# Performance work log

Measured on AMD Instinct MI355X. Metric: run time of the kernel, lower is better.

The kernel has to match this reference:

```python
import jax, jax.numpy as jnp
import numpy as np

N_NODES = 50000
N_EDGES = 800000
C_IN = 32          # in_channels
N_RAD = 8          # num_radial gaussians
RBF_START, RBF_STOP = 0.0, 5.0


def setup_inputs() -> dict:
    key = jax.random.key(0)
    ks = jax.random.split(key, 8)
    x = jax.random.normal(ks[0], (N_NODES, C_IN), dtype=jnp.float32)
    pos = jax.random.normal(ks[1], (N_NODES, 3), dtype=jnp.float32)
    edge_index = jax.random.randint(ks[2], (2, N_EDGES), 0, N_NODES, dtype=jnp.int64)
    # Xavier-uniform-style init for weights
    def xavier(k, shape, fan_in, fan_out):
        lim = np.sqrt(6.0 / (fan_in + fan_out))
        return jax.random.uniform(k, shape, minval=-lim, maxval=lim, dtype=jnp.float32)
    W_tp = xavier(ks[3], (C_IN, N_RAD, C_IN), C_IN, N_RAD * C_IN)
    W1 = xavier(ks[4], (N_RAD * C_IN, C_IN), N_RAD * C_IN, C_IN)
    b1 = jnp.zeros((C_IN,), dtype=jnp.float32)
    W2 = xavier(ks[5], (C_IN, C_IN), C_IN, C_IN)
    b2 = jnp.zeros((C_IN,), dtype=jnp.float32)
    return {"x": x, "pos": pos, "edge_index": edge_index,
            "W_tp": W_tp, "W1": W1, "b1": b1, "W2": W2, "b2": b2}


def _gaussian_smearing(dist):
    # dist: (E,) -> (E, N_RAD)
    centers = jnp.linspace(RBF_START, RBF_STOP, N_RAD)  # (R,)
    width = (RBF_STOP - RBF_START) / (N_RAD - 1)
    scaling = 1.0 / jnp.sqrt(2.0 * jnp.pi)
    d = dist[:, None] - centers[None, :]
    return scaling * jnp.exp(-0.5 * (d / width) ** 2)


def reference(x, pos, edge_index, W_tp, W1, b1, W2, b2):
    row = edge_index[0]  # target (central) nodes
    col = edge_index[1]  # source (neighbor) nodes
    # edge geometry
    edge_vector = pos[row] - pos[col]                       # (E, 3)
    dist = jnp.sqrt(jnp.sum(edge_vector * edge_vector, axis=-1) + 1e-12)  # (E,)
    rbf = _gaussian_smearing(dist)                          # (E, R)
    # tensor product: gather neighbor features, weight by radial basis
    x_j = x[col]                                            # (E, C)
    weighted = jnp.einsum('ec,cro->ero', x_j, W_tp)         # (E, R, C)
    tp = weighted * rbf[:, :, None]                         # (E, R, C)
    # per-edge MLP on flattened tensor-product output
    msg = tp.reshape(tp.shape[0], -1)                       # (E, R*C)
    msg = jax.nn.silu(msg @ W1 + b1)                        # (E, C)
    msg = msg @ W2 + b2                                     # (E, C)
    # scatter-add messages to central nodes, residual update
    agg = jax.ops.segment_sum(msg, row, num_segments=x.shape[0])  # (N, C)
    return x + agg
```

## Files before the change

kernel.cpp:

```cpp
#include <hip/hip_runtime.h>
#include <hip/hip_bf16.h>

#define C 32
#define R 8
#define NPB 32
#define K_ELL 32
#define OVF_CAP 65536

typedef unsigned int u32;
__device__ __forceinline__ float bflo(u32 u) { return __uint_as_float(u << 16); }
__device__ __forceinline__ float bfhi(u32 u) { return __uint_as_float(u & 0xffff0000u); }
__device__ __forceinline__ u32 f2bf_bits(float f) {
    u32 u = __float_as_uint(f);
    u32 lsb = (u >> 16) & 1u;
    return (u + 0x7fffu + lsb) >> 16;
}

__global__ void k_prepM(const float* __restrict__ Wtp, const float* __restrict__ W1,
                        float* __restrict__ M) {
    int idx = blockIdx.x * 256 + threadIdx.x;
    if (idx >= R * C * C) return;
    int r = idx >> 10;
    int c = (idx >> 5) & 31;
    int j = idx & 31;
    float acc = 0.f;
#pragma unroll
    for (int o = 0; o < C; ++o)
        acc = fmaf(Wtp[c * R * C + r * C + o], W1[(r * C + o) * C + j], acc);
    M[idx] = acc;
}

__global__ void k_fused(const float* __restrict__ x, const float* __restrict__ M,
                        __hip_bfloat16* __restrict__ z,
                        const int* __restrict__ ei, const float* __restrict__ pos,
                        int* __restrict__ cnt, int* __restrict__ ovfcnt,
                        uint4* __restrict__ ovf,
                        u32* __restrict__ ell, int N, int E, int ZB) {
    __shared__ float xs[NPB * C];
    int t = threadIdx.x;
    if ((int)blockIdx.x < ZB) {
        int n0 = blockIdx.x * NPB;
        for (int i = t * 4; i < NPB * C; i += 256 * 4) {
            size_t gbase = (size_t)n0 * C + i;
            float4 v = make_float4(0.f, 0.f, 0.f, 0.f);
            if (gbase + 3 < (size_t)N * C) v = *(const float4*)(x + gbase);
            *(float4*)(xs + i) = v;
        }
        __syncthreads();
        int r = t & 7, j = t >> 3;
        float m[C];
#pragma unroll
        for (int c = 0; c < C; ++c) m[c] = M[r * C * C + c * C + j];
        int nmax = N - n0; if (nmax > NPB) nmax = NPB;
        for (int nn = 0; nn < nmax; ++nn) {
            const float* xp = xs + nn * C;
            float acc = 0.f;
#pragma unroll
            for (int c = 0; c < C; ++c) acc = fmaf(xp[c], m[c], acc);
            z[(size_t)(n0 + nn) * (R * C) + t] = __float2bfloat16(acc);
        }
    } else {
        int i = (blockIdx.x - ZB) * 256 + t;
        if (i < E) {
            int r = ei[i];
            int c = ei[E + i];
            r = ((unsigned)r < (unsigned)N) ? r : 0;
            c = ((unsigned)c < (unsigned)N) ? c : 0;
            float dx = pos[r * 3 + 0] - pos[c * 3 + 0];
            float dy = pos[r * 3 + 1] - pos[c * 3 + 1];
            float dz = pos[r * 3 + 2] - pos[c * 3 + 2];
            float dist = sqrtf(fmaf(dx, dx, fmaf(dy, dy, dz * dz)) + 1e-12f);
            int local = atomicAdd(&cnt[r], 1);
            if (local < K_ELL) {
                ell[(size_t)r * K_ELL + local] = (u32)c | (f2bf_bits(dist) << 16);
            } else {
                int q = atomicAdd(ovfcnt, 1);
                if (q < OVF_CAP)
                    ovf[q] = make_uint4((u32)r, (u32)c, __float_as_uint(dist), 0u);
            }
        }
    }
}

__device__ __forceinline__ float silu_f(float h) {
    return h * __builtin_amdgcn_rcpf(1.f + __expf(-h));
}

__device__ __forceinline__ float rbf_dot(float d, uint4 zv, float b1j) {
    const float Einv = 0.36787944f;
    float u = 1.3999999f * d;
    float f = 0.3989423f * __expf(-0.5f * u * u);
    float t = __expf(u - 0.5f);
    float h = fmaf(f, bflo(zv.x), b1j);
    f *= t;            h = fmaf(f, bfhi(zv.x), h);
    t *= Einv; f *= t; h = fmaf(f, bflo(zv.y), h);
    t *= Einv; f *= t; h = fmaf(f, bfhi(zv.y), h);
    t *= Einv; f *= t; h = fmaf(f, bflo(zv.z), h);
    t *= Einv; f *= t; h = fmaf(f, bfhi(zv.z), h);
    t *= Einv; f *= t; h = fmaf(f, bflo(zv.w), h);
    t *= Einv; f *= t; h = fmaf(f, bfhi(zv.w), h);
    return h;
}

__global__ void k_edge_ell(const int* __restrict__ cnt, const u32* __restrict__ ell,
                           const __hip_bfloat16* __restrict__ z,
                           const float* __restrict__ x, const float* __restrict__ b1,
                           const float* __restrict__ W2, const float* __restrict__ b2,
                           float* __restrict__ out, int N) {
    __shared__ float W2s[C * C];
    for (int i = threadIdx.x; i < C * C; i += blockDim.x) W2s[i] = W2[i];
    __syncthreads();
    int gt = blockIdx.x * blockDim.x + threadIdx.x;
    int j = gt & 31;
    int n = gt >> 5;
    if (n >= N) return;
    int deg = cnt[n];
    int m = deg < K_ELL ? deg : K_ELL;
    u32 packv = 0u;
    if (j < m) packv = ell[(size_t)n * K_ELL + j];
    float b1j = b1[j];
    float acc = 0.f;
    int base = 0;
    for (; base + 4 <= m; base += 4) {
        u32 w0 = __shfl(packv, base + 0, 32);
        u32 w1 = __shfl(packv, base + 1, 32);
        u32 w2 = __shfl(packv, base + 2, 32);
        u32 w3 = __shfl(packv, base + 3, 32);
        uint4 z0 = ((const uint4*)(z + (size_t)(w0 & 0xffffu) * (R * C)))[j];
        uint4 z1 = ((const uint4*)(z + (size_t)(w1 & 0xffffu) * (R * C)))[j];
        uint4 z2 = ((const uint4*)(z + (size_t)(w2 & 0xffffu) * (R * C)))[j];
        uint4 z3 = ((const uint4*)(z + (size_t)(w3 & 0xffffu) * (R * C)))[j];
        float h0 = rbf_dot(__uint_as_float(w0 & 0xffff0000u), z0, b1j);
        float h1 = rbf_dot(__uint_as_float(w1 & 0xffff0000u), z1, b1j);
        float h2 = rbf_dot(__uint_as_float(w2 & 0xffff0000u), z2, b1j);
        float h3 = rbf_dot(__uint_as_float(w3 & 0xffff0000u), z3, b1j);
        acc += silu_f(h0) + silu_f(h1) + silu_f(h2) + silu_f(h3);
    }
    for (; base < m; ++base) {
        u32 w0 = __shfl(packv, base, 32);
        uint4 z0 = ((const uint4*)(z + (size_t)(w0 & 0xffffu) * (R * C)))[j];
        acc += silu_f(rbf_dot(__uint_as_float(w0 & 0xffff0000u), z0, b1j));
    }
    float v = fmaf((float)deg, b2[j], x[(size_t)n * C + j]);
#pragma unroll
    for (int i = 0; i < C; ++i)
        v = fmaf(__shfl(acc, i, 32), W2s[i * C + j], v);
    out[(size_t)n * C + j] = v;
}

__global__ void k_overflow(const int* __restrict__ ovfcnt, const uint4* __restrict__ ovf,
                           const __hip_bfloat16* __restrict__ z,
                           const float* __restrict__ b1, const float* __restrict__ W2,
                           float* __restrict__ out, int N) {
    int novf = ovfcnt[0];
    if (novf > OVF_CAP) novf = OVF_CAP;
    int gt = blockIdx.x * blockDim.x + threadIdx.x;
    int j = gt & 31;
    int g = gt >> 5;
    int ngroups = (gridDim.x * blockDim.x) >> 5;
    for (int q = g; q < novf; q += ngroups) {
        uint4 rec = ovf[q];
        u32 row = rec.x, col = rec.y;
        float dist = __uint_as_float(rec.z);
        uint4 zv = ((const uint4*)(z + (size_t)col * (R * C)))[j];
        float sh = silu_f(rbf_dot(dist, zv, b1[j]));
        float v = 0.f;
#pragma unroll
        for (int i = 0; i < C; ++i)
            v = fmaf(__shfl(sh, i, 32), W2[i * C + j], v);
        atomicAdd(&out[(size_t)row * C + j], v);
    }
}

__device__ __forceinline__ float rbf_lane(float dist, int r) {
    float t = (dist - 0.71428573f * (float)r) * 1.3999999f;
    return 0.3989423f * __expf(-0.5f * t * t);
}

__global__ void k_edge_direct(const int* __restrict__ ei, const float* __restrict__ pos,
                              const float* __restrict__ x, const float* __restrict__ M,
                              const float* __restrict__ b1,
                              float* __restrict__ agg, float* __restrict__ deg,
                              int E, int N) {
    __shared__ float Ms[R * C * C];
    for (int i = threadIdx.x; i < R * C * C; i += blockDim.x) Ms[i] = M[i];
    __syncthreads();
    int gt = blockIdx.x * blockDim.x + threadIdx.x;
    int j = gt & 31;
    int g = gt >> 5;
    int ngroups = (gridDim.x * blockDim.x) >> 5;
    float b1j = b1[j];
    for (int e = g; e < E; e += ngroups) {
        int row = ei[e];
        int col = ei[E + e];
        row = ((unsigned)row < (unsigned)N) ? row : 0;
        col = ((unsigned)col < (unsigned)N) ? col : 0;
        float dx = pos[row * 3 + 0] - pos[col * 3 + 0];
        float dy = pos[row * 3 + 1] - pos[col * 3 + 1];
        float dz = pos[row * 3 + 2] - pos[col * 3 + 2];
        float dist = sqrtf(fmaf(dx, dx, fmaf(dy, dy, dz * dz)) + 1e-12f);
        float my_rbf = rbf_lane(dist, j & 7);
        float xr[C];
#pragma unroll
        for (int c = 0; c < C; ++c) xr[c] = x[(size_t)col * C + c];
        float h = b1j;
#pragma unroll
        for (int r = 0; r < R; ++r) {
            float s = 0.f;
#pragma unroll
            for (int c = 0; c < C; ++c)
                s = fmaf(xr[c], Ms[r * C * C + c * C + j], s);
            h = fmaf(__shfl(my_rbf, r, 32), s, h);
        }
        float sh = h / (1.f + __expf(-h));
        atomicAdd(&agg[(size_t)row * C + j], sh);
        if (j == 0) atomicAdd(&deg[row], 1.f);
    }
}

__global__ void k_final(const float* __restrict__ x, const float* __restrict__ agg,
                        const float* __restrict__ deg, const float* __restrict__ W2,
                        const float* __restrict__ b2, float* __restrict__ out,
                        int N) {
    int t = threadIdx.x;
    int j = t & 31;
    float w2[C];
#pragma unroll
    for (int i = 0; i < C; ++i) w2[i] = W2[i * C + j];
    float b2j = b2[j];
    int g = (blockIdx.x * blockDim.x + t) >> 5;
    int ngroups = (gridDim.x * blockDim.x) >> 5;
    for (int n = g; n < N; n += ngroups) {
        const float* ap = agg + (size_t)n * C;
        float acc = 0.f;
#pragma unroll
        for (int i = 0; i < C; ++i) acc = fmaf(ap[i], w2[i], acc);
        out[(size_t)n * C + j] = x[(size_t)n * C + j] + acc + deg[n] * b2j;
    }
}

__global__ void k_edge_full(const int* __restrict__ ei, const float* __restrict__ pos,
                            const float* __restrict__ x,
                            const float* __restrict__ Wtp, const float* __restrict__ W1,
                            const float* __restrict__ b1,
                            const float* __restrict__ W2, const float* __restrict__ b2,
                            float* __restrict__ out, int E, int N) {
    __shared__ float Ms[R * C * C];
    __shared__ float W2s[C * C];
    for (int idx = threadIdx.x; idx < R * C * C; idx += blockDim.x) {
        int r = idx >> 10, c = (idx >> 5) & 31, jj = idx & 31;
        float acc = 0.f;
#pragma unroll
        for (int o = 0; o < C; ++o)
            acc = fmaf(Wtp[c * R * C + r * C + o], W1[(r * C + o) * C + jj], acc);
        Ms[idx] = acc;
    }
    for (int idx = threadIdx.x; idx < C * C; idx += blockDim.x) W2s[idx] = W2[idx];
    __syncthreads();
    int gt = blockIdx.x * blockDim.x + threadIdx.x;
    int j = gt & 31;
    int g = gt >> 5;
    int ngroups = (gridDim.x * blockDim.x) >> 5;
    float b1j = b1[j];
    float b2j = b2[j];
    for (int e = g; e < E; e += ngroups) {
        int row = ei[e];
        int col = ei[E + e];
        row = ((unsigned)row < (unsigned)N) ? row : 0;
        col = ((unsigned)col < (unsigned)N) ? col : 0;
        float dx = pos[row * 3 + 0] - pos[col * 3 + 0];
        float dy = pos[row * 3 + 1] - pos[col * 3 + 1];
        float dz = pos[row * 3 + 2] - pos[col * 3 + 2];
        float dist = sqrtf(fmaf(dx, dx, fmaf(dy, dy, dz * dz)) + 1e-12f);
        float my_rbf = rbf_lane(dist, j & 7);
        float xr[C];
#pragma unroll
        for (int c = 0; c < C; ++c) xr[c] = x[(size_t)col * C + c];
        float h = b1j;
#pragma unroll
        for (int r = 0; r < R; ++r) {
            float s = 0.f;
#pragma unroll
            for (int c = 0; c < C; ++c)
                s = fmaf(xr[c], Ms[r * C * C + c * C + j], s);
            h = fmaf(__shfl(my_rbf, r, 32), s, h);
        }
        float sh = h / (1.f + __expf(-h));
        float v = b2j;
#pragma unroll
        for (int i = 0; i < C; ++i)
            v = fmaf(__shfl(sh, i, 32), W2s[i * C + j], v);
        atomicAdd(&out[(size_t)row * C + j], v);
    }
}

__global__ void k_add_x(const float* __restrict__ x, float* __restrict__ out, int total) {
    int i = blockIdx.x * blockDim.x + threadIdx.x;
    int stride = gridDim.x * blockDim.x;
    for (; i < total; i += stride) out[i] += x[i];
}

extern "C" void kernel_launch(void* const* d_in, const int* in_sizes, int n_in,
                              void* d_out, int out_size, void* d_ws, size_t ws_size,
                              hipStream_t stream) {
    const float* x   = (const float*)d_in[0];
    const float* pos = (const float*)d_in[1];
    const int*   ei  = (const int*)d_in[2];
    const float* Wtp = (const float*)d_in[3];
    const float* W1  = (const float*)d_in[4];
    const float* b1  = (const float*)d_in[5];
    const float* W2  = (const float*)d_in[6];
    const float* b2  = (const float*)d_in[7];
    int N = in_sizes[0] / C;
    int E = in_sizes[2] / 2;

    char* ws = (char*)d_ws;
    size_t mBytes   = (size_t)R * C * C * sizeof(float);
    size_t zBytes   = (size_t)N * R * C * sizeof(__hip_bfloat16);
    size_t cntB     = (size_t)N * sizeof(int);
    size_t ovfcB    = 64;
    size_t ovfB     = (size_t)OVF_CAP * 16;
    size_t ellB     = (size_t)N * K_ELL * sizeof(u32);
    size_t aggBytes = (size_t)N * (C + 1) * sizeof(float);
    size_t tierANeed = mBytes + zBytes + cntB + ovfcB + ovfB + ellB;
    bool tierA = (ws_size >= tierANeed) && (N <= 65535);
    bool tierB = !tierA && ws_size >= mBytes + aggBytes;

    if (tierA) {
        size_t off = 0;
        float*          M      = (float*)(ws + off); off += mBytes;
        __hip_bfloat16* z      = (__hip_bfloat16*)(ws + off); off += zBytes;
        int*            cnt    = (int*)(ws + off); off += cntB;
        int*            ovfcnt = (int*)(ws + off); off += ovfcB;
        uint4*          ovf    = (uint4*)(ws + off); off += ovfB;
        u32*            ell    = (u32*)(ws + off);

        hipMemsetAsync(cnt, 0, cntB + ovfcB, stream);
        k_prepM<<<(R * C * C + 255) / 256, 256, 0, stream>>>(Wtp, W1, M);
        int ZB = (N + NPB - 1) / NPB;
        int SB = (E + 255) / 256;
        k_fused<<<ZB + SB, 256, 0, stream>>>(x, M, z, ei, pos, cnt, ovfcnt, ovf,
                                             ell, N, E, ZB);
        int blocks = (int)(((size_t)N * 32 + 255) / 256);
        k_edge_ell<<<blocks, 256, 0, stream>>>(cnt, ell, z, x, b1, W2, b2,
                                               (float*)d_out, N);
        k_overflow<<<16, 256, 0, stream>>>(ovfcnt, ovf, z, b1, W2,
                                           (float*)d_out, N);
    } else if (tierB) {
        float* M   = (float*)ws;
        float* agg = (float*)(ws + mBytes);
        float* deg = agg + (size_t)N * C;
        hipMemsetAsync(agg, 0, aggBytes, stream);
        k_prepM<<<(R * C * C + 255) / 256, 256, 0, stream>>>(Wtp, W1, M);
        k_edge_direct<<<2048, 256, 0, stream>>>(ei, pos, x, M, b1, agg, deg, E, N);
        k_final<<<1024, 256, 0, stream>>>(x, agg, deg, W2, b2, (float*)d_out, N);
    } else {
        hipMemsetAsync(d_out, 0, (size_t)N * C * sizeof(float), stream);
        k_edge_full<<<1024, 256, 0, stream>>>(ei, pos, x, Wtp, W1, b1, W2, b2,
                                              (float*)d_out, E, N);
        k_add_x<<<1024, 256, 0, stream>>>(x, (float*)d_out, N * C);
    }
}
```

Measured before the change: 128.7 us.

## Move edge distance computation into gather kernel using padded float4 positions

The scatter stage no longer gathers positions or computes distances. It only writes 16-bit neighbor indices into the ELL table and 8-byte overflow records, which cuts random pos reads and ELL bytes on the atomic-heavy scatter path. A new block group in the fused kernel copies pos into a float4 array, and the ELL consumer computes distances on the fly from pos4[n] and pos4[col]. That adds a 16-byte random gather per edge in the consumer but removes the bf16 rounding of dist.

```diff
diff --git a/kernel.cpp b/kernel.cpp
--- a/kernel.cpp
+++ b/kernel.cpp
@@ -8,13 +8,9 @@
 #define OVF_CAP 65536
 
 typedef unsigned int u32;
+typedef unsigned short u16;
 __device__ __forceinline__ float bflo(u32 u) { return __uint_as_float(u << 16); }
 __device__ __forceinline__ float bfhi(u32 u) { return __uint_as_float(u & 0xffff0000u); }
-__device__ __forceinline__ u32 f2bf_bits(float f) {
-    u32 u = __float_as_uint(f);
-    u32 lsb = (u >> 16) & 1u;
-    return (u + 0x7fffu + lsb) >> 16;
-}
 
 __global__ void k_prepM(const float* __restrict__ Wtp, const float* __restrict__ W1,
                         float* __restrict__ M) {
@@ -33,13 +29,25 @@
 __global__ void k_fused(const float* __restrict__ x, const float* __restrict__ M,
                         __hip_bfloat16* __restrict__ z,
                         const int* __restrict__ ei, const float* __restrict__ pos,
+                        float4* __restrict__ pos4,
                         int* __restrict__ cnt, int* __restrict__ ovfcnt,
-                        uint4* __restrict__ ovf,
-                        u32* __restrict__ ell, int N, int E, int ZB) {
+                        uint2* __restrict__ ovf,
+                        u16* __restrict__ ell, int N, int E, int PB, int ZB) {
     __shared__ float xs[NPB * C];
     int t = threadIdx.x;
-    if ((int)blockIdx.x < ZB) {
-        int n0 = blockIdx.x * NPB;
+    int bid = blockIdx.x;
+    if (bid < PB) {
+        int n = bid * 256 + t;
+        if (n < N) {
+            float4 p;
+            p.x = pos[n * 3 + 0];
+            p.y = pos[n * 3 + 1];
+            p.z = pos[n * 3 + 2];
+            p.w = 0.f;
+            pos4[n] = p;
+        }
+    } else if (bid < PB + ZB) {
+        int n0 = (bid - PB) * NPB;
         for (int i = t * 4; i < NPB * C; i += 256 * 4) {
             size_t gbase = (size_t)n0 * C + i;
             float4 v = make_float4(0.f, 0.f, 0.f, 0.f);
@@ -60,23 +68,18 @@
             z[(size_t)(n0 + nn) * (R * C) + t] = __float2bfloat16(acc);
         }
     } else {
-        int i = (blockIdx.x - ZB) * 256 + t;
+        int i = (bid - PB - ZB) * 256 + t;
         if (i < E) {
             int r = ei[i];
             int c = ei[E + i];
             r = ((unsigned)r < (unsigned)N) ? r : 0;
             c = ((unsigned)c < (unsigned)N) ? c : 0;
-            float dx = pos[r * 3 + 0] - pos[c * 3 + 0];
-            float dy = pos[r * 3 + 1] - pos[c * 3 + 1];
-            float dz = pos[r * 3 + 2] - pos[c * 3 + 2];
-            float dist = sqrtf(fmaf(dx, dx, fmaf(dy, dy, dz * dz)) + 1e-12f);
             int local = atomicAdd(&cnt[r], 1);
             if (local < K_ELL) {
-                ell[(size_t)r * K_ELL + local] = (u32)c | (f2bf_bits(dist) << 16);
+                ell[(size_t)r * K_ELL + local] = (u16)c;
             } else {
                 int q = atomicAdd(ovfcnt, 1);
-                if (q < OVF_CAP)
-                    ovf[q] = make_uint4((u32)r, (u32)c, __float_as_uint(dist), 0u);
+                if (q < OVF_CAP) ovf[q] = make_uint2((u32)r, (u32)c);
             }
         }
     }
@@ -102,8 +105,14 @@
     return h;
 }
 
-__global__ void k_edge_ell(const int* __restrict__ cnt, const u32* __restrict__ ell,
+__device__ __forceinline__ float dist_f(float4 a, float4 b) {
+    float dx = a.x - b.x, dy = a.y - b.y, dz = a.z - b.z;
+    return sqrtf(fmaf(dx, dx, fmaf(dy, dy, dz * dz)) + 1e-12f);
+}
+
+__global__ void k_edge_ell(const int* __restrict__ cnt, const u16* __restrict__ ell,
                            const __hip_bfloat16* __restrict__ z,
+                           const float4* __restrict__ pos4,
                            const float* __restrict__ x, const float* __restrict__ b1,
                            const float* __restrict__ W2, const float* __restrict__ b2,
                            float* __restrict__ out, int N) {
@@ -116,30 +125,35 @@
     if (n >= N) return;
     int deg = cnt[n];
     int m = deg < K_ELL ? deg : K_ELL;
-    u32 packv = 0u;
-    if (j < m) packv = ell[(size_t)n * K_ELL + j];
+    int mycol = (j < m) ? (int)ell[(size_t)n * K_ELL + j] : 0;
+    float4 pr = pos4[n];
     float b1j = b1[j];
     float acc = 0.f;
     int base = 0;
     for (; base + 4 <= m; base += 4) {
-        u32 w0 = __shfl(packv, base + 0, 32);
-        u32 w1 = __shfl(packv, base + 1, 32);
-        u32 w2 = __shfl(packv, base + 2, 32);
-        u32 w3 = __shfl(packv, base + 3, 32);
-        uint4 z0 = ((const uint4*)(z + (size_t)(w0 & 0xffffu) * (R * C)))[j];
-        uint4 z1 = ((const uint4*)(z + (size_t)(w1 & 0xffffu) * (R * C)))[j];
-        uint4 z2 = ((const uint4*)(z + (size_t)(w2 & 0xffffu) * (R * C)))[j];
-        uint4 z3 = ((const uint4*)(z + (size_t)(w3 & 0xffffu) * (R * C)))[j];
-        float h0 = rbf_dot(__uint_as_float(w0 & 0xffff0000u), z0, b1j);
-        float h1 = rbf_dot(__uint_as_float(w1 & 0xffff0000u), z1, b1j);
-        float h2 = rbf_dot(__uint_as_float(w2 & 0xffff0000u), z2, b1j);
-        float h3 = rbf_dot(__uint_as_float(w3 & 0xffff0000u), z3, b1j);
+        int c0 = __shfl(mycol, base + 0, 32);
+        int c1 = __shfl(mycol, base + 1, 32);
+        int c2 = __shfl(mycol, base + 2, 32);
+        int c3 = __shfl(mycol, base + 3, 32);
+        float4 q0 = pos4[c0];
+        float4 q1 = pos4[c1];
+        float4 q2 = pos4[c2];
+        float4 q3 = pos4[c3];
+        uint4 z0 = ((const uint4*)(z + (size_t)c0 * (R * C)))[j];
+        uint4 z1 = ((const uint4*)(z + (size_t)c1 * (R * C)))[j];
+        uint4 z2 = ((const uint4*)(z + (size_t)c2 * (R * C)))[j];
+        uint4 z3 = ((const uint4*)(z + (size_t)c3 * (R * C)))[j];
+        float h0 = rbf_dot(dist_f(pr, q0), z0, b1j);
+        float h1 = rbf_dot(dist_f(pr, q1), z1, b1j);
+        float h2 = rbf_dot(dist_f(pr, q2), z2, b1j);
+        float h3 = rbf_dot(dist_f(pr, q3), z3, b1j);
         acc += silu_f(h0) + silu_f(h1) + silu_f(h2) + silu_f(h3);
     }
     for (; base < m; ++base) {
-        u32 w0 = __shfl(packv, base, 32);
-        uint4 z0 = ((const uint4*)(z + (size_t)(w0 & 0xffffu) * (R * C)))[j];
-        acc += silu_f(rbf_dot(__uint_as_float(w0 & 0xffff0000u), z0, b1j));
+        int c0 = __shfl(mycol, base, 32);
+        float4 q0 = pos4[c0];
+        uint4 z0 = ((const uint4*)(z + (size_t)c0 * (R * C)))[j];
+        acc += silu_f(rbf_dot(dist_f(pr, q0), z0, b1j));
     }
     float v = fmaf((float)deg, b2[j], x[(size_t)n * C + j]);
 #pragma unroll
@@ -148,8 +162,9 @@
     out[(size_t)n * C + j] = v;
 }
 
-__global__ void k_overflow(const int* __restrict__ ovfcnt, const uint4* __restrict__ ovf,
+__global__ void k_overflow(const int* __restrict__ ovfcnt, const uint2* __restrict__ ovf,
                            const __hip_bfloat16* __restrict__ z,
+                           const float4* __restrict__ pos4,
                            const float* __restrict__ b1, const float* __restrict__ W2,
                            float* __restrict__ out, int N) {
     int novf = ovfcnt[0];
@@ -159,9 +174,9 @@
     int g = gt >> 5;
     int ngroups = (gridDim.x * blockDim.x) >> 5;
     for (int q = g; q < novf; q += ngroups) {
-        uint4 rec = ovf[q];
-        u32 row = rec.x, col = rec.y;
-        float dist = __uint_as_float(rec.z);
+        uint2 rec = ovf[q];
+        int row = (int)rec.x, col = (int)rec.y;
+        float dist = dist_f(pos4[row], pos4[col]);
         uint4 zv = ((const uint4*)(z + (size_t)col * (R * C)))[j];
         float sh = silu_f(rbf_dot(dist, zv, b1[j]));
         float v = 0.f;
@@ -319,10 +334,11 @@
     size_t zBytes   = (size_t)N * R * C * sizeof(__hip_bfloat16);
     size_t cntB     = (size_t)N * sizeof(int);
     size_t ovfcB    = 64;
-    size_t ovfB     = (size_t)OVF_CAP * 16;
-    size_t ellB     = (size_t)N * K_ELL * sizeof(u32);
+    size_t ovfB     = (size_t)OVF_CAP * 8;
+    size_t ellB     = (size_t)N * K_ELL * sizeof(u16);
+    size_t pos4B    = (size_t)N * sizeof(float4);
     size_t aggBytes = (size_t)N * (C + 1) * sizeof(float);
-    size_t tierANeed = mBytes + zBytes + cntB + ovfcB + ovfB + ellB;
+    size_t tierANeed = mBytes + zBytes + cntB + ovfcB + ovfB + ellB + pos4B;
     bool tierA = (ws_size >= tierANeed) && (N <= 65535);
     bool tierB = !tierA && ws_size >= mBytes + aggBytes;
 
@@ -332,19 +348,21 @@
         __hip_bfloat16* z      = (__hip_bfloat16*)(ws + off); off += zBytes;
         int*            cnt    = (int*)(ws + off); off += cntB;
         int*            ovfcnt = (int*)(ws + off); off += ovfcB;
-        uint4*          ovf    = (uint4*)(ws + off); off += ovfB;
-        u32*            ell    = (u32*)(ws + off);
+        uint2*          ovf    = (uint2*)(ws + off); off += ovfB;
+        u16*            ell    = (u16*)(ws + off); off += ellB;
+        float4*         pos4   = (float4*)(ws + off);
 
         hipMemsetAsync(cnt, 0, cntB + ovfcB, stream);
         k_prepM<<<(R * C * C + 255) / 256, 256, 0, stream>>>(Wtp, W1, M);
+        int PB = (N + 255) / 256;
         int ZB = (N + NPB - 1) / NPB;
         int SB = (E + 255) / 256;
-        k_fused<<<ZB + SB, 256, 0, stream>>>(x, M, z, ei, pos, cnt, ovfcnt, ovf,
-                                             ell, N, E, ZB);
+        k_fused<<<PB + ZB + SB, 256, 0, stream>>>(x, M, z, ei, pos, pos4, cnt,
+                                                  ovfcnt, ovf, ell, N, E, PB, ZB);
         int blocks = (int)(((size_t)N * 32 + 255) / 256);
-        k_edge_ell<<<blocks, 256, 0, stream>>>(cnt, ell, z, x, b1, W2, b2,
+        k_edge_ell<<<blocks, 256, 0, stream>>>(cnt, ell, z, pos4, x, b1, W2, b2,
                                                (float*)d_out, N);
-        k_overflow<<<16, 256, 0, stream>>>(ovfcnt, ovf, z, b1, W2,
+        k_overflow<<<16, 256, 0, stream>>>(ovfcnt, ovf, z, pos4, b1, W2,
                                            (float*)d_out, N);
     } else if (tierB) {
         float* M   = (float*)ws;
```

Result: slower. 163.1 us (+26.7%).

## Two-pass bucketed scatter of edges into ELL to localize atomics

Applied to the files above, without the earlier changes.

Instead of each edge thread atomically appending directly into a random per-node ELL slot, edges are first binned by destination-row range into 8 global buckets via shared-memory staging, then a new kernel scatters each bucket into the ELL. The aim is better cache locality for the cnt atomics and ELL writes, since each bucket covers about 1/8 of the nodes. The cost is an extra kernel launch plus a round-trip write and read of 8 bytes per edge, along with more shared memory in the fused kernel, which may lower occupancy for its z-compute blocks. Edge order within ELL rows changes, so floating-point summation order may differ.

```diff
diff --git a/kernel.cpp b/kernel.cpp
--- a/kernel.cpp
+++ b/kernel.cpp
@@ -6,6 +6,7 @@
 #define NPB 32
 #define K_ELL 32
 #define OVF_CAP 65536
+#define NBKT 8
 
 typedef unsigned int u32;
 __device__ __forceinline__ float bflo(u32 u) { return __uint_as_float(u << 16); }
@@ -34,9 +35,13 @@
                         __hip_bfloat16* __restrict__ z,
                         const int* __restrict__ ei, const float* __restrict__ pos,
                         int* __restrict__ cnt, int* __restrict__ ovfcnt,
-                        uint4* __restrict__ ovf,
-                        u32* __restrict__ ell, int N, int E, int ZB) {
+                        int* __restrict__ gbcnt, uint4* __restrict__ ovf,
+                        uint2* __restrict__ bucket, u32* __restrict__ ell,
+                        int N, int E, int ZB, int RPB8, int CAP) {
     __shared__ float xs[NPB * C];
+    __shared__ u32 s_rc[NBKT * 256];
+    __shared__ u32 s_d[NBKT * 256];
+    __shared__ int lcnt[NBKT], lbase[NBKT];
     int t = threadIdx.x;
     if ((int)blockIdx.x < ZB) {
         int n0 = blockIdx.x * NPB;
@@ -60,6 +65,8 @@
             z[(size_t)(n0 + nn) * (R * C) + t] = __float2bfloat16(acc);
         }
     } else {
+        if (t < NBKT) lcnt[t] = 0;
+        __syncthreads();
         int i = (blockIdx.x - ZB) * 256 + t;
         if (i < E) {
             int r = ei[i];
@@ -70,15 +77,55 @@
             float dy = pos[r * 3 + 1] - pos[c * 3 + 1];
             float dz = pos[r * 3 + 2] - pos[c * 3 + 2];
             float dist = sqrtf(fmaf(dx, dx, fmaf(dy, dy, dz * dz)) + 1e-12f);
-            int local = atomicAdd(&cnt[r], 1);
-            if (local < K_ELL) {
-                ell[(size_t)r * K_ELL + local] = (u32)c | (f2bf_bits(dist) << 16);
-            } else {
-                int q = atomicAdd(ovfcnt, 1);
-                if (q < OVF_CAP)
-                    ovf[q] = make_uint4((u32)r, (u32)c, __float_as_uint(dist), 0u);
+            int k = r / RPB8;
+            int slot = atomicAdd(&lcnt[k], 1);
+            s_rc[k * 256 + slot] = (u32)r | ((u32)c << 16);
+            s_d[k * 256 + slot]  = __float_as_uint(dist);
+        }
+        __syncthreads();
+        if (t < NBKT) lbase[t] = atomicAdd(&gbcnt[t], lcnt[t]);
+        __syncthreads();
+        for (int kk = 0; kk < NBKT; ++kk) {
+            int ck = lcnt[kk];
+            if (t < ck) {
+                int p = lbase[kk] + t;
+                u32 rcv = s_rc[kk * 256 + t];
+                u32 db  = s_d[kk * 256 + t];
+                if (p < CAP) {
+                    uint2 rec; rec.x = rcv; rec.y = db;
+                    bucket[(size_t)kk * CAP + p] = rec;
+                } else {
+                    int r = rcv & 0xffff, c = (int)(rcv >> 16);
+                    float dist = __uint_as_float(db);
+                    int local = atomicAdd(&cnt[r], 1);
+                    if (local < K_ELL)
+                        ell[(size_t)r * K_ELL + local] = (u32)c | (f2bf_bits(dist) << 16);
+                    else {
+                        int q = atomicAdd(ovfcnt, 1);
+                        if (q < OVF_CAP) ovf[q] = make_uint4((u32)r, (u32)c, db, 0u);
+                    }
+                }
             }
         }
+    }
+}
+
+__global__ void k_scatter2(const uint2* __restrict__ bucket, const int* __restrict__ gbcnt,
+                           int* __restrict__ cnt, int* __restrict__ ovfcnt,
+                           uint4* __restrict__ ovf, u32* __restrict__ ell, int CAP) {
+    int k = blockIdx.x & (NBKT - 1);
+    int idx = (int)(blockIdx.x >> 3) * 256 + threadIdx.x;
+    int cn = gbcnt[k]; if (cn > CAP) cn = CAP;
+    if (idx >= cn) return;
+    uint2 rec = bucket[(size_t)k * CAP + idx];
+    int r = rec.x & 0xffff, c = (int)(rec.x >> 16);
+    float dist = __uint_as_float(rec.y);
+    int local = atomicAdd(&cnt[r], 1);
+    if (local < K_ELL) {
+        ell[(size_t)r * K_ELL + local] = (u32)c | (f2bf_bits(dist) << 16);
+    } else {
+        int q = atomicAdd(ovfcnt, 1);
+        if (q < OVF_CAP) ovf[q] = make_uint4((u32)r, (u32)c, rec.y, 0u);
     }
 }
 
@@ -315,14 +362,16 @@
     int E = in_sizes[2] / 2;
 
     char* ws = (char*)d_ws;
+    int CAP = E / NBKT + 16384;
     size_t mBytes   = (size_t)R * C * C * sizeof(float);
     size_t zBytes   = (size_t)N * R * C * sizeof(__hip_bfloat16);
     size_t cntB     = (size_t)N * sizeof(int);
-    size_t ovfcB    = 64;
+    size_t ctrlB    = 64;
     size_t ovfB     = (size_t)OVF_CAP * 16;
     size_t ellB     = (size_t)N * K_ELL * sizeof(u32);
+    size_t bktB     = (size_t)NBKT * CAP * sizeof(uint2);
     size_t aggBytes = (size_t)N * (C + 1) * sizeof(float);
-    size_t tierANeed = mBytes + zBytes + cntB + ovfcB + ovfB + ellB;
+    size_t tierANeed = mBytes + zBytes + cntB + ctrlB + ovfB + ellB + bktB;
     bool tierA = (ws_size >= tierANeed) && (N <= 65535);
     bool tierB = !tierA && ws_size >= mBytes + aggBytes;
 
@@ -331,16 +380,23 @@
         float*          M      = (float*)(ws + off); off += mBytes;
         __hip_bfloat16* z      = (__hip_bfloat16*)(ws + off); off += zBytes;
         int*            cnt    = (int*)(ws + off); off += cntB;
-        int*            ovfcnt = (int*)(ws + off); off += ovfcB;
+        int*            ctrl   = (int*)(ws + off); off += ctrlB;
         uint4*          ovf    = (uint4*)(ws + off); off += ovfB;
-        u32*            ell    = (u32*)(ws + off);
-
-        hipMemsetAsync(cnt, 0, cntB + ovfcB, stream);
+        u32*            ell    = (u32*)(ws + off); off += ellB;
+        uint2*          bucket = (uint2*)(ws + off);
+        int* ovfcnt = ctrl;
+        int* gbcnt  = ctrl + 1;
+
+        hipMemsetAsync(cnt, 0, cntB + ctrlB, stream);
         k_prepM<<<(R * C * C + 255) / 256, 256, 0, stream>>>(Wtp, W1, M);
+        int RPB8 = (N + NBKT - 1) / NBKT;
         int ZB = (N + NPB - 1) / NPB;
         int SB = (E + 255) / 256;
-        k_fused<<<ZB + SB, 256, 0, stream>>>(x, M, z, ei, pos, cnt, ovfcnt, ovf,
-                                             ell, N, E, ZB);
+        k_fused<<<ZB + SB, 256, 0, stream>>>(x, M, z, ei, pos, cnt, ovfcnt, gbcnt,
+                                             ovf, bucket, ell, N, E, ZB, RPB8, CAP);
+        int s2blocks = ((CAP + 255) / 256) * NBKT;
+        k_scatter2<<<s2blocks, 256, 0, stream>>>(bucket, gbcnt, cnt, ovfcnt, ovf,
+                                                 ell, CAP);
         int blocks = (int)(((size_t)N * 32 + 255) / 256);
         k_edge_ell<<<blocks, 256, 0, stream>>>(cnt, ell, z, x, b1, W2, b2,
                                                (float*)d_out, N);
```

Measured after the change: 165.0 us. 28.1% more time.
